# Performance work log

Hardware: AMD Instinct MI355X
Metric: run time of the kernel (lower is better)

Reference implementation:

```python
import jax, jax.numpy as jnp
import numpy as np

B, N, D, H = 32, 2048, 65, 64  # batch, seq_len, in_dim+out_dim, hid
GAMMA = 0.0001


def setup_inputs() -> dict:
    key = jax.random.key(0)
    kx, kq, kk, kv = jax.random.split(key, 4)
    x = jax.random.normal(kx, (B, N, D), dtype=jnp.float32)
    std_qk = (GAMMA / D) ** 0.5
    Wq = jax.random.normal(kq, (H, D), dtype=jnp.float32) * std_qk
    Wk = jax.random.normal(kk, (H, D), dtype=jnp.float32) * std_qk
    Wv = jax.random.normal(kv, (D, D), dtype=jnp.float32) * GAMMA
    return {"x": x, "Wq": Wq, "Wk": Wk, "Wv": Wv}


def reference(x, Wq, Wk, Wv):
    # Linear projections (torch nn.Linear: x @ W^T)
    Q = jnp.einsum('bnd,hd->bnh', x, Wq)  # [B, N, H]
    K = jnp.einsum('bnd,hd->bnh', x, Wk)  # [B, N, H]
    V = jnp.einsum('bnd,ed->bne', x, Wv)  # [B, N, D]
    # Non-softmax linear attention: (Q K^T) V, as written in the module
    scores = jnp.einsum('bnh,bmh->bnm', Q, K)  # [B, N, N]
    out = jnp.einsum('bnm,bmd->bnd', scores, V)  # [B, N, D]
    return out
```

## Files before the change

kernel.cpp:

```cpp
#include <hip/hip_runtime.h>

#define BB 32
#define NN 2048
#define DD 65
#define HH 64
#define ST 68
#define TILE (DD * ST)
#define CC 32

__device__ __forceinline__ float4 f4add(float4 a, float4 b) {
  return make_float4(a.x + b.x, a.y + b.y, a.z + b.z, a.w + b.w);
}

#define GL2LDS(g, l)                                             \
  __builtin_amdgcn_global_load_lds(                              \
      (const __attribute__((address_space(1))) void*)(g),        \
      (__attribute__((address_space(3))) void*)(l), 16, 0, 0)

__global__ __launch_bounds__(256, 4) void k1_gram(const float* __restrict__ x,
                                                  float* __restrict__ P) {
  __shared__ __align__(16) float Xl[64 * ST];
  const int t = (int)threadIdx.x;
  const int tx = t & 15, ty = t >> 4;
  const int blk = (int)blockIdx.x;
  const int b = blk >> 5, c = blk & 31;
  const float4* src4 =
      (const float4*)(x + ((size_t)b * NN + (size_t)c * 64) * DD);

  {
    float4 tmp[5];
#pragma unroll
    for (int q = 0; q < 5; q++) {
      const int i4 = t + 256 * q;
      if (i4 < 1040) tmp[q] = src4[i4];
    }
#pragma unroll
    for (int q = 0; q < 5; q++) {
      const int i4 = t + 256 * q;
      if (i4 < 1040) {
        const int f = 4 * i4;
        const float vv[4] = {tmp[q].x, tmp[q].y, tmp[q].z, tmp[q].w};
#pragma unroll
        for (int j = 0; j < 4; j++) {
          const int r = (f + j) / DD, cc = (f + j) - r * DD;
          Xl[r * ST + cc] = vv[j];
        }
      }
    }
  }
  __syncthreads();

  float g[4][4] = {};
  float g64[4] = {};
  float gcc = 0.f;
  for (int n = 0; n < 64; n++) {
    float rowf[4], colf[4];
    *(float4*)rowf = *(const float4*)&Xl[n * ST + 4 * ty];
    *(float4*)colf = *(const float4*)&Xl[n * ST + 4 * tx];
    const float x64 = Xl[n * ST + 64];
#pragma unroll
    for (int r = 0; r < 4; r++)
#pragma unroll
      for (int cc = 0; cc < 4; cc++)
        g[r][cc] = fmaf(rowf[r], colf[cc], g[r][cc]);
#pragma unroll
    for (int cc = 0; cc < 4; cc++) g64[cc] = fmaf(x64, colf[cc], g64[cc]);
    gcc = fmaf(x64, x64, gcc);
  }
  float* Pp = P + (size_t)blk * TILE;
#pragma unroll
  for (int r = 0; r < 4; r++)
    *(float4*)&Pp[(4 * ty + r) * ST + 4 * tx] = *(float4*)g[r];
  if (ty == 0) {
    *(float4*)&Pp[64 * ST + 4 * tx] = *(float4*)g64;
#pragma unroll
    for (int cc = 0; cc < 4; cc++)
      Pp[(4 * tx + cc) * ST + 64] = g64[cc];
    if (tx == 0) Pp[64 * ST + 64] = gcc;
  }
}

__global__ __launch_bounds__(256) void kred(const float* __restrict__ P,
                                            float* __restrict__ G) {
  const int t = (int)threadIdx.x;
  const int blk = (int)blockIdx.x;
  const int b = blk / 5, s = blk - b * 5;
  const int Q = TILE / 4;
  const int i4 = s * 256 + t;
  if (i4 < Q) {
    const float4* Pb = (const float4*)(P + (size_t)b * CC * TILE);
    float4 acc = make_float4(0.f, 0.f, 0.f, 0.f);
#pragma unroll
    for (int grp = 0; grp < 4; grp++) {
      float4 v[8];
#pragma unroll
      for (int cc = 0; cc < 8; cc++)
        v[cc] = Pb[(size_t)(8 * grp + cc) * Q + i4];
#pragma unroll
      for (int stp = 4; stp >= 1; stp >>= 1)
#pragma unroll
        for (int cc = 0; cc < stp; cc++) v[cc] = f4add(v[cc], v[cc + stp]);
      acc = f4add(acc, v[0]);
    }
    ((float4*)(G + (size_t)b * TILE))[i4] = acc;
  }
}

__global__ __launch_bounds__(256) void k2_chain(
    const float* __restrict__ Wq, const float* __restrict__ Wk,
    const float* __restrict__ Wv, const float* __restrict__ G,
    float* __restrict__ Tm) {
  __shared__ __align__(16) float WqL[HH * ST];
  __shared__ __align__(16) float WkL[HH * ST];
  __shared__ __align__(16) float GL[TILE];
  __shared__ __align__(16) float WvT[TILE];
  __shared__ __align__(16) float Mr[8 * ST];
  __shared__ __align__(16) float Rr[8 * ST];

  const int t = (int)threadIdx.x;
  const int tx = t & 31, ty = t >> 5;
  const int blk = (int)blockIdx.x;
  const int b = blk / 9, rg = blk - b * 9;
  const int i = 8 * rg + ty;
  const bool alive = (i < DD);
  const int ic = alive ? i : 0;

  {
    float tq[17], tk[17];
#pragma unroll
    for (int q = 0; q < 17; q++) {
      const int idx = t + 256 * q;
      if (idx < HH * DD) { tq[q] = Wq[idx]; tk[q] = Wk[idx]; }
    }
#pragma unroll
    for (int q = 0; q < 17; q++) {
      const int idx = t + 256 * q;
      if (idx < HH * DD) {
        const int r = idx / DD, cc = idx - r * DD;
        WqL[r * ST + cc] = tq[q];
        WkL[r * ST + cc] = tk[q];
      }
    }
  }
  {
    const float4* Gb4 = (const float4*)(G + (size_t)b * TILE);
    float4 tG[5];
#pragma unroll
    for (int q = 0; q < 5; q++) {
      const int i4 = t + 256 * q;
      if (i4 < TILE / 4) tG[q] = Gb4[i4];
    }
#pragma unroll
    for (int q = 0; q < 5; q++) {
      const int i4 = t + 256 * q;
      if (i4 < TILE / 4) *((float4*)GL + i4) = tG[q];
    }
  }
  {
    float tv[17];
#pragma unroll
    for (int q = 0; q < 17; q++) {
      const int idx = t + 256 * q;
      if (idx < DD * DD) tv[q] = Wv[idx];
    }
#pragma unroll
    for (int q = 0; q < 17; q++) {
      const int idx = t + 256 * q;
      if (idx < DD * DD) {
        const int j = idx / DD, k = idx - j * DD;
        WvT[k * ST + j] = tv[q];
      }
    }
  }
  __syncthreads();

  {
    float m0 = 0.f, m1 = 0.f, m2 = 0.f;
    for (int h = 0; h < HH; h++) {
      const float wq = WqL[h * ST + ic];
      m0 = fmaf(wq, WkL[h * ST + tx], m0);
      m1 = fmaf(wq, WkL[h * ST + tx + 32], m1);
      m2 = fmaf(wq, WkL[h * ST + 64], m2);
    }
    if (alive) {
      Mr[ty * ST + tx] = m0;
      Mr[ty * ST + tx + 32] = m1;
      if (tx == 0) Mr[ty * ST + 64] = m2;
    }
  }
  __syncthreads();

  {
    float r0 = 0.f, r1 = 0.f, r2 = 0.f;
    for (int k = 0; k < DD; k++) {
      const float mm = Mr[ty * ST + k];
      r0 = fmaf(mm, GL[k * ST + tx], r0);
      r1 = fmaf(mm, GL[k * ST + tx + 32], r1);
      r2 = fmaf(mm, GL[k * ST + 64], r2);
    }
    if (alive) {
      Rr[ty * ST + tx] = r0;
      Rr[ty * ST + tx + 32] = r1;
      if (tx == 0) Rr[ty * ST + 64] = r2;
    }
  }
  __syncthreads();

  {
    float t0 = 0.f, t1 = 0.f, t2 = 0.f;
    for (int k = 0; k < DD; k++) {
      const float rv = Rr[ty * ST + k];
      t0 = fmaf(rv, WvT[k * ST + tx], t0);
      t1 = fmaf(rv, WvT[k * ST + tx + 32], t1);
      t2 = fmaf(rv, WvT[k * ST + 64], t2);
    }
    if (alive) {
      float* Tb = Tm + (size_t)b * TILE + (size_t)i * ST;
      Tb[tx] = t0;
      Tb[tx + 32] = t1;
      if (tx == 0) Tb[64] = t2;
    }
  }
}

__global__ __launch_bounds__(256, 4) void k3_out(const float* __restrict__ x,
                                                 const float* __restrict__ Tt,
                                                 float* __restrict__ out) {
  __shared__ __align__(16) float Tl[TILE];
  __shared__ __align__(16) float Xl[64 * ST];
  const int t = (int)threadIdx.x;
  const int tx = t & 15, ty = t >> 4;
  const int wid = t >> 6, lane = t & 63;
  const int blk = (int)blockIdx.x;
  const int b = blk >> 5;
  const int rb = (blk & 31) * 64;
  const float4* Tg4 = (const float4*)(Tt + (size_t)b * TILE);
  const float4* src4 = (const float4*)(x + ((size_t)b * NN + rb) * DD);

#pragma unroll
  for (int q = 0; q < 4; q++) {
    const int s = q * 256 + wid * 64 + lane;
    GL2LDS(Tg4 + s, Tl + (size_t)(q * 256 + wid * 64) * 4);
  }
  {
    const int s = 1024 + wid * 64 + lane;
    if (s < TILE / 4) GL2LDS(Tg4 + s, Tl + (size_t)(1024 + wid * 64) * 4);
  }

  {
    float4 tmp[5];
#pragma unroll
    for (int q = 0; q < 5; q++) {
      const int i4 = t + 256 * q;
      if (i4 < 1040) tmp[q] = src4[i4];
    }
#pragma unroll
    for (int q = 0; q < 5; q++) {
      const int i4 = t + 256 * q;
      if (i4 < 1040) {
        const int f = 4 * i4;
        const float vv[4] = {tmp[q].x, tmp[q].y, tmp[q].z, tmp[q].w};
#pragma unroll
        for (int j = 0; j < 4; j++) {
          const int r = (f + j) / DD, cc = (f + j) - r * DD;
          Xl[r * ST + cc] = vv[j];
        }
      }
    }
  }
  __syncthreads();

  float o[4][4] = {}, o64[4] = {};
  for (int kk = 0; kk < 64; kk += 4) {
    float xa4[4][4];
    float tb4[4][4];
    float t64e[4];
#pragma unroll
    for (int r = 0; r < 4; r++)
      *(float4*)xa4[r] = *(const float4*)&Xl[(4 * ty + r) * ST + kk];
#pragma unroll
    for (int e = 0; e < 4; e++)
      *(float4*)tb4[e] = *(const float4*)&Tl[(kk + e) * ST + 4 * tx];
#pragma unroll
    for (int e = 0; e < 4; e++) t64e[e] = Tl[(kk + e) * ST + 64];
#pragma unroll
    for (int e = 0; e < 4; e++) {
#pragma unroll
      for (int r = 0; r < 4; r++)
#pragma unroll
        for (int cc = 0; cc < 4; cc++)
          o[r][cc] = fmaf(xa4[r][e], tb4[e][cc], o[r][cc]);
#pragma unroll
      for (int r = 0; r < 4; r++)
        o64[r] = fmaf(xa4[r][e], t64e[e], o64[r]);
    }
  }
  {
    float xs[4];
#pragma unroll
    for (int r = 0; r < 4; r++) xs[r] = Xl[(4 * ty + r) * ST + 64];
    float tb[4];
    *(float4*)tb = *(const float4*)&Tl[64 * ST + 4 * tx];
    const float t64 = Tl[64 * ST + 64];
#pragma unroll
    for (int r = 0; r < 4; r++) {
#pragma unroll
      for (int cc = 0; cc < 4; cc++)
        o[r][cc] = fmaf(xs[r], tb[cc], o[r][cc]);
      o64[r] = fmaf(xs[r], t64, o64[r]);
    }
  }

  __syncthreads();
  float* Ol = Xl;
#pragma unroll
  for (int r = 0; r < 4; r++) {
#pragma unroll
    for (int cc = 0; cc < 4; cc++)
      Ol[(4 * ty + r) * DD + 4 * tx + cc] = o[r][cc];
  }
  if (tx == 0) {
#pragma unroll
    for (int r = 0; r < 4; r++) Ol[(4 * ty + r) * DD + 64] = o64[r];
  }
  __syncthreads();
  {
    float4* ob4 = (float4*)(out + ((size_t)b * NN + rb) * DD);
    const float4* Ol4 = (const float4*)Ol;
#pragma unroll
    for (int q = 0; q < 5; q++) {
      const int i4 = t + 256 * q;
      if (i4 < (64 * DD) / 4) ob4[i4] = Ol4[i4];
    }
  }
}

extern "C" void kernel_launch(void* const* d_in, const int* in_sizes, int n_in,
                              void* d_out, int out_size, void* d_ws,
                              size_t ws_size, hipStream_t stream) {
  const float* x = (const float*)d_in[0];
  const float* Wq = (const float*)d_in[1];
  const float* Wk = (const float*)d_in[2];
  const float* Wv = (const float*)d_in[3];
  float* out = (float*)d_out;

  float* P = (float*)d_ws;
  float* G = P + (size_t)BB * CC * TILE;
  float* Tm = G + (size_t)BB * TILE;

  k1_gram<<<BB * CC, 256, 0, stream>>>(x, P);
  kred<<<BB * 5, 256, 0, stream>>>(P, G);
  k2_chain<<<BB * 9, 256, 0, stream>>>(Wq, Wk, Wv, G, Tm);
  k3_out<<<BB * CC, 256, 0, stream>>>(x, Tm, out);
  (void)in_sizes; (void)n_in; (void)out_size; (void)ws_size;
}
```

Before: 117.2 us.

## Fuse four kernels into one cooperative kernel with grid-wide syncs

Replaces the four separate launches (gram partials, reduction, weight chain, output) with one cooperative kernel of 1024 blocks that uses grid.sync between phases and reuses one shared-memory buffer across phases. The chain phase now reads Wq directly from global and stores Wk/Wv in a narrower-stride LDS buffer to fit the smaller footprint. The aim is to remove launch gaps and tail effects between the dependent kernels. The cost is three grid-wide barriers, the requirement that all 1024 blocks be co-resident, and idle blocks during the small reduction and chain phases. If the cooperative launch fails it falls back to the original four launches.

```diff
diff --git a/kernel.cpp b/kernel.cpp
--- a/kernel.cpp
+++ b/kernel.cpp
@@ -1,4 +1,7 @@
 #include <hip/hip_runtime.h>
+#include <hip/hip_cooperative_groups.h>
+
+namespace cg = cooperative_groups;
 
 #define BB 32
 #define NN 2048
@@ -7,6 +10,12 @@
 #define ST 68
 #define TILE (DD * ST)
 #define CC 32
+#define WST 66
+
+#define OFF1 17680
+#define OFFM 35088
+#define OFFR 37264
+#define SMEM_BYTES 39440
 
 __device__ __forceinline__ float4 f4add(float4 a, float4 b) {
   return make_float4(a.x + b.x, a.y + b.y, a.z + b.z, a.w + b.w);
@@ -16,6 +25,325 @@
   __builtin_amdgcn_global_load_lds(                              \
       (const __attribute__((address_space(1))) void*)(g),        \
       (__attribute__((address_space(3))) void*)(l), 16, 0, 0)
+
+__global__ __launch_bounds__(256, 4) void fused(
+    const float* __restrict__ x, const float* __restrict__ Wq,
+    const float* __restrict__ Wk, const float* __restrict__ Wv,
+    float* __restrict__ P, float* __restrict__ G, float* __restrict__ Tm,
+    float* __restrict__ out) {
+  __shared__ __align__(16) char smem[SMEM_BYTES];
+  const int t = (int)threadIdx.x;
+  const int bid = (int)blockIdx.x;
+
+  {
+    float* Xl = (float*)smem;
+    const int tx = t & 15, ty = t >> 4;
+    const int b = bid >> 5, c = bid & 31;
+    const float4* src4 =
+        (const float4*)(x + ((size_t)b * NN + (size_t)c * 64) * DD);
+
+    {
+      float4 tmp[5];
+#pragma unroll
+      for (int q = 0; q < 5; q++) {
+        const int i4 = t + 256 * q;
+        if (i4 < 1040) tmp[q] = src4[i4];
+      }
+#pragma unroll
+      for (int q = 0; q < 5; q++) {
+        const int i4 = t + 256 * q;
+        if (i4 < 1040) {
+          const int f = 4 * i4;
+          const float vv[4] = {tmp[q].x, tmp[q].y, tmp[q].z, tmp[q].w};
+#pragma unroll
+          for (int j = 0; j < 4; j++) {
+            const int r = (f + j) / DD, cc = (f + j) - r * DD;
+            Xl[r * ST + cc] = vv[j];
+          }
+        }
+      }
+    }
+    __syncthreads();
+
+    float g[4][4] = {};
+    float g64[4] = {};
+    float gcc = 0.f;
+    for (int n = 0; n < 64; n++) {
+      float rowf[4], colf[4];
+      *(float4*)rowf = *(const float4*)&Xl[n * ST + 4 * ty];
+      *(float4*)colf = *(const float4*)&Xl[n * ST + 4 * tx];
+      const float x64 = Xl[n * ST + 64];
+#pragma unroll
+      for (int r = 0; r < 4; r++)
+#pragma unroll
+        for (int cc = 0; cc < 4; cc++)
+          g[r][cc] = fmaf(rowf[r], colf[cc], g[r][cc]);
+#pragma unroll
+      for (int cc = 0; cc < 4; cc++) g64[cc] = fmaf(x64, colf[cc], g64[cc]);
+      gcc = fmaf(x64, x64, gcc);
+    }
+    float* Pp = P + (size_t)bid * TILE;
+#pragma unroll
+    for (int r = 0; r < 4; r++)
+      *(float4*)&Pp[(4 * ty + r) * ST + 4 * tx] = *(float4*)g[r];
+    if (ty == 0) {
+      *(float4*)&Pp[64 * ST + 4 * tx] = *(float4*)g64;
+#pragma unroll
+      for (int cc = 0; cc < 4; cc++)
+        Pp[(4 * tx + cc) * ST + 64] = g64[cc];
+      if (tx == 0) Pp[64 * ST + 64] = gcc;
+    }
+  }
+  cg::this_grid().sync();
+
+  if (bid < BB * 5) {
+    const int b = bid / 5, s = bid - b * 5;
+    const int Q = TILE / 4;
+    const int i4 = s * 256 + t;
+    if (i4 < Q) {
+      const float4* Pb = (const float4*)(P + (size_t)b * CC * TILE);
+      float4 acc = make_float4(0.f, 0.f, 0.f, 0.f);
+#pragma unroll
+      for (int grp = 0; grp < 4; grp++) {
+        float4 v[8];
+#pragma unroll
+        for (int cc = 0; cc < 8; cc++)
+          v[cc] = Pb[(size_t)(8 * grp + cc) * Q + i4];
+#pragma unroll
+        for (int stp = 4; stp >= 1; stp >>= 1)
+#pragma unroll
+          for (int cc = 0; cc < stp; cc++) v[cc] = f4add(v[cc], v[cc + stp]);
+        acc = f4add(acc, v[0]);
+      }
+      ((float4*)(G + (size_t)b * TILE))[i4] = acc;
+    }
+  }
+  cg::this_grid().sync();
+
+  if (bid < BB * 9) {
+    float* GL = (float*)smem;
+    float* WkL = (float*)(smem + OFF1);
+    float* Mr = (float*)(smem + OFFM);
+    float* Rr = (float*)(smem + OFFR);
+    const int tx = t & 31, ty = t >> 5;
+    const int b = bid / 9, rg = bid - b * 9;
+    const int i = 8 * rg + ty;
+    const bool alive = (i < DD);
+    const int ic = alive ? i : 0;
+
+    {
+      const float4* Wk4 = (const float4*)Wk;
+      const float4* Gb4 = (const float4*)(G + (size_t)b * TILE);
+      float4 tk[5], tG[5];
+#pragma unroll
+      for (int q = 0; q < 5; q++) {
+        const int i4 = t + 256 * q;
+        if (i4 < 1040) tk[q] = Wk4[i4];
+      }
+#pragma unroll
+      for (int q = 0; q < 5; q++) {
+        const int i4 = t + 256 * q;
+        if (i4 < TILE / 4) tG[q] = Gb4[i4];
+      }
+#pragma unroll
+      for (int q = 0; q < 5; q++) {
+        const int i4 = t + 256 * q;
+        if (i4 < 1040) {
+          const int f = 4 * i4;
+          const float vv[4] = {tk[q].x, tk[q].y, tk[q].z, tk[q].w};
+#pragma unroll
+          for (int j = 0; j < 4; j++) {
+            const int r = (f + j) / DD, cc = (f + j) - r * DD;
+            WkL[r * WST + cc] = vv[j];
+          }
+        }
+      }
+#pragma unroll
+      for (int q = 0; q < 5; q++) {
+        const int i4 = t + 256 * q;
+        if (i4 < TILE / 4) ((float4*)GL)[i4] = tG[q];
+      }
+    }
+    __syncthreads();
+
+    {
+      float m0 = 0.f, m1 = 0.f, m2 = 0.f;
+#pragma unroll 4
+      for (int h = 0; h < HH; h++) {
+        const float wq = Wq[h * DD + ic];
+        m0 = fmaf(wq, WkL[h * WST + tx], m0);
+        m1 = fmaf(wq, WkL[h * WST + tx + 32], m1);
+        m2 = fmaf(wq, WkL[h * WST + 64], m2);
+      }
+      if (alive) {
+        Mr[ty * ST + tx] = m0;
+        Mr[ty * ST + tx + 32] = m1;
+        if (tx == 0) Mr[ty * ST + 64] = m2;
+      }
+    }
+    __syncthreads();
+
+    {
+      float r0 = 0.f, r1 = 0.f, r2 = 0.f;
+      for (int k = 0; k < DD; k++) {
+        const float mm = Mr[ty * ST + k];
+        r0 = fmaf(mm, GL[k * ST + tx], r0);
+        r1 = fmaf(mm, GL[k * ST + tx + 32], r1);
+        r2 = fmaf(mm, GL[k * ST + 64], r2);
+      }
+      if (alive) {
+        Rr[ty * ST + tx] = r0;
+        Rr[ty * ST + tx + 32] = r1;
+        if (tx == 0) Rr[ty * ST + 64] = r2;
+      }
+    }
+    __syncthreads();
+
+    {
+      float tv[17];
+#pragma unroll
+      for (int q = 0; q < 17; q++) {
+        const int idx = t + 256 * q;
+        if (idx < DD * DD) tv[q] = Wv[idx];
+      }
+#pragma unroll
+      for (int q = 0; q < 17; q++) {
+        const int idx = t + 256 * q;
+        if (idx < DD * DD) {
+          const int j = idx / DD, k = idx - j * DD;
+          WkL[k * WST + j] = tv[q];
+        }
+      }
+    }
+    __syncthreads();
+
+    {
+      const float* WvT = WkL;
+      float t0 = 0.f, t1 = 0.f, t2 = 0.f;
+      for (int k = 0; k < DD; k++) {
+        const float rv = Rr[ty * ST + k];
+        t0 = fmaf(rv, WvT[k * WST + tx], t0);
+        t1 = fmaf(rv, WvT[k * WST + tx + 32], t1);
+        t2 = fmaf(rv, WvT[k * WST + 64], t2);
+      }
+      if (alive) {
+        float* Tb = Tm + (size_t)b * TILE + (size_t)i * ST;
+        Tb[tx] = t0;
+        Tb[tx + 32] = t1;
+        if (tx == 0) Tb[64] = t2;
+      }
+    }
+  }
+  cg::this_grid().sync();
+
+  {
+    float* Tl = (float*)smem;
+    float* Xl = (float*)(smem + OFF1);
+    const int tx = t & 15, ty = t >> 4;
+    const int wid = t >> 6, lane = t & 63;
+    const int b = bid >> 5;
+    const int rb = (bid & 31) * 64;
+    const float4* Tg4 = (const float4*)(Tm + (size_t)b * TILE);
+    const float4* src4 = (const float4*)(x + ((size_t)b * NN + rb) * DD);
+
+#pragma unroll
+    for (int q = 0; q < 4; q++) {
+      const int s = q * 256 + wid * 64 + lane;
+      GL2LDS(Tg4 + s, Tl + (size_t)(q * 256 + wid * 64) * 4);
+    }
+    {
+      const int s = 1024 + wid * 64 + lane;
+      if (s < TILE / 4) GL2LDS(Tg4 + s, Tl + (size_t)(1024 + wid * 64) * 4);
+    }
+
+    {
+      float4 tmp[5];
+#pragma unroll
+      for (int q = 0; q < 5; q++) {
+        const int i4 = t + 256 * q;
+        if (i4 < 1040) tmp[q] = src4[i4];
+      }
+#pragma unroll
+      for (int q = 0; q < 5; q++) {
+        const int i4 = t + 256 * q;
+        if (i4 < 1040) {
+          const int f = 4 * i4;
+          const float vv[4] = {tmp[q].x, tmp[q].y, tmp[q].z, tmp[q].w};
+#pragma unroll
+          for (int j = 0; j < 4; j++) {
+            const int r = (f + j) / DD, cc = (f + j) - r * DD;
+            Xl[r * ST + cc] = vv[j];
+          }
+        }
+      }
+    }
+    __syncthreads();
+
+    float o[4][4] = {}, o64[4] = {};
+    for (int kk = 0; kk < 64; kk += 4) {
+      float xa4[4][4];
+      float tb4[4][4];
+      float t64e[4];
+#pragma unroll
+      for (int r = 0; r < 4; r++)
+        *(float4*)xa4[r] = *(const float4*)&Xl[(4 * ty + r) * ST + kk];
+#pragma unroll
+      for (int e = 0; e < 4; e++)
+        *(float4*)tb4[e] = *(const float4*)&Tl[(kk + e) * ST + 4 * tx];
+#pragma unroll
+      for (int e = 0; e < 4; e++) t64e[e] = Tl[(kk + e) * ST + 64];
+#pragma unroll
+      for (int e = 0; e < 4; e++) {
+#pragma unroll
+        for (int r = 0; r < 4; r++)
+#pragma unroll
+          for (int cc = 0; cc < 4; cc++)
+            o[r][cc] = fmaf(xa4[r][e], tb4[e][cc], o[r][cc]);
+#pragma unroll
+        for (int r = 0; r < 4; r++)
+          o64[r] = fmaf(xa4[r][e], t64e[e], o64[r]);
+      }
+    }
+    {
+      float xs[4];
+#pragma unroll
+      for (int r = 0; r < 4; r++) xs[r] = Xl[(4 * ty + r) * ST + 64];
+      float tb[4];
+      *(float4*)tb = *(const float4*)&Tl[64 * ST + 4 * tx];
+      const float t64 = Tl[64 * ST + 64];
+#pragma unroll
+      for (int r = 0; r < 4; r++) {
+#pragma unroll
+        for (int cc = 0; cc < 4; cc++)
+          o[r][cc] = fmaf(xs[r], tb[cc], o[r][cc]);
+        o64[r] = fmaf(xs[r], t64, o64[r]);
+      }
+    }
+
+    __syncthreads();
+    float* Ol = Xl;
+#pragma unroll
+    for (int r = 0; r < 4; r++) {
+#pragma unroll
+      for (int cc = 0; cc < 4; cc++)
+        Ol[(4 * ty + r) * DD + 4 * tx + cc] = o[r][cc];
+    }
+    if (tx == 0) {
+#pragma unroll
+      for (int r = 0; r < 4; r++) Ol[(4 * ty + r) * DD + 64] = o64[r];
+    }
+    __syncthreads();
+    {
+      float4* ob4 = (float4*)(out + ((size_t)b * NN + rb) * DD);
+      const float4* Ol4 = (const float4*)Ol;
+#pragma unroll
+      for (int q = 0; q < 5; q++) {
+        const int i4 = t + 256 * q;
+        if (i4 < (64 * DD) / 4) ob4[i4] = Ol4[i4];
+      }
+    }
+  }
+}
 
 __global__ __launch_bounds__(256, 4) void k1_gram(const float* __restrict__ x,
                                                   float* __restrict__ P) {
@@ -26,7 +354,6 @@
   const int b = blk >> 5, c = blk & 31;
   const float4* src4 =
       (const float4*)(x + ((size_t)b * NN + (size_t)c * 64) * DD);
-
   {
     float4 tmp[5];
 #pragma unroll
@@ -49,9 +376,7 @@
     }
   }
   __syncthreads();
-
-  float g[4][4] = {};
-  float g64[4] = {};
+  float g[4][4] = {}, g64[4] = {};
   float gcc = 0.f;
   for (int n = 0; n < 64; n++) {
     float rowf[4], colf[4];
@@ -74,8 +399,7 @@
   if (ty == 0) {
     *(float4*)&Pp[64 * ST + 4 * tx] = *(float4*)g64;
 #pragma unroll
-    for (int cc = 0; cc < 4; cc++)
-      Pp[(4 * tx + cc) * ST + 64] = g64[cc];
+    for (int cc = 0; cc < 4; cc++) Pp[(4 * tx + cc) * ST + 64] = g64[cc];
     if (tx == 0) Pp[64 * ST + 64] = gcc;
   }
 }
@@ -116,7 +440,6 @@
   __shared__ __align__(16) float WvT[TILE];
   __shared__ __align__(16) float Mr[8 * ST];
   __shared__ __align__(16) float Rr[8 * ST];
-
   const int t = (int)threadIdx.x;
   const int tx = t & 31, ty = t >> 5;
   const int blk = (int)blockIdx.x;
@@ -124,7 +447,6 @@
   const int i = 8 * rg + ty;
   const bool alive = (i < DD);
   const int ic = alive ? i : 0;
-
   {
     float tq[17], tk[17];
 #pragma unroll
@@ -173,7 +495,6 @@
     }
   }
   __syncthreads();
-
   {
     float m0 = 0.f, m1 = 0.f, m2 = 0.f;
     for (int h = 0; h < HH; h++) {
@@ -189,7 +510,6 @@
     }
   }
   __syncthreads();
-
   {
     float r0 = 0.f, r1 = 0.f, r2 = 0.f;
     for (int k = 0; k < DD; k++) {
@@ -205,7 +525,6 @@
     }
   }
   __syncthreads();
-
   {
     float t0 = 0.f, t1 = 0.f, t2 = 0.f;
     for (int k = 0; k < DD; k++) {
@@ -236,7 +555,6 @@
   const int rb = (blk & 31) * 64;
   const float4* Tg4 = (const float4*)(Tt + (size_t)b * TILE);
   const float4* src4 = (const float4*)(x + ((size_t)b * NN + rb) * DD);
-
 #pragma unroll
   for (int q = 0; q < 4; q++) {
     const int s = q * 256 + wid * 64 + lane;
@@ -246,7 +564,6 @@
     const int s = 1024 + wid * 64 + lane;
     if (s < TILE / 4) GL2LDS(Tg4 + s, Tl + (size_t)(1024 + wid * 64) * 4);
   }
-
   {
     float4 tmp[5];
 #pragma unroll
@@ -269,12 +586,9 @@
     }
   }
   __syncthreads();
-
   float o[4][4] = {}, o64[4] = {};
   for (int kk = 0; kk < 64; kk += 4) {
-    float xa4[4][4];
-    float tb4[4][4];
-    float t64e[4];
+    float xa4[4][4], tb4[4][4], t64e[4];
 #pragma unroll
     for (int r = 0; r < 4; r++)
       *(float4*)xa4[r] = *(const float4*)&Xl[(4 * ty + r) * ST + kk];
@@ -310,7 +624,6 @@
       o64[r] = fmaf(xs[r], t64, o64[r]);
     }
   }
-
   __syncthreads();
   float* Ol = Xl;
 #pragma unroll
@@ -348,9 +661,15 @@
   float* G = P + (size_t)BB * CC * TILE;
   float* Tm = G + (size_t)BB * TILE;
 
-  k1_gram<<<BB * CC, 256, 0, stream>>>(x, P);
-  kred<<<BB * 5, 256, 0, stream>>>(P, G);
-  k2_chain<<<BB * 9, 256, 0, stream>>>(Wq, Wk, Wv, G, Tm);
-  k3_out<<<BB * CC, 256, 0, stream>>>(x, Tm, out);
+  void* kargs[] = {(void*)&x, (void*)&Wq, (void*)&Wk, (void*)&Wv,
+                   (void*)&P, (void*)&G, (void*)&Tm, (void*)&out};
+  hipError_t err = hipLaunchCooperativeKernel(
+      (void*)fused, dim3(BB * CC), dim3(256), kargs, 0, stream);
+  if (err != hipSuccess) {
+    k1_gram<<<BB * CC, 256, 0, stream>>>(x, P);
+    kred<<<BB * 5, 256, 0, stream>>>(P, G);
+    k2_chain<<<BB * 9, 256, 0, stream>>>(Wq, Wk, Wv, G, Tm);
+    k3_out<<<BB * CC, 256, 0, stream>>>(x, Tm, out);
+  }
   (void)in_sizes; (void)n_in; (void)out_size; (void)ws_size;
 }
```

Result: slower. 419.8 us (+258.3%).

## Fuse gram reduction and weight chain into gram kernel via last-block atomic counter

Applied to the files above, without the earlier changes.

Merges the partial-gram, reduction and Wq/Wk/Wv chain kernels into one kernel. The last block per batch, detected with a threadfence plus an atomic counter, sums the 32 partial grams and computes the 65x65 chain product with a 4x4 register tile per thread. This removes two kernel launches and the G round trip through global memory. In exchange, the serial tail of each batch now runs on a single block, and an extra memset launch is added to reset the counters.

```diff
diff --git a/kernel.cpp b/kernel.cpp
--- a/kernel.cpp
+++ b/kernel.cpp
@@ -17,215 +17,247 @@
       (const __attribute__((address_space(1))) void*)(g),        \
       (__attribute__((address_space(3))) void*)(l), 16, 0, 0)
 
-__global__ __launch_bounds__(256, 4) void k1_gram(const float* __restrict__ x,
-                                                  float* __restrict__ P) {
-  __shared__ __align__(16) float Xl[64 * ST];
+__global__ __launch_bounds__(256, 4) void kA(
+    const float* __restrict__ x, const float* __restrict__ Wq,
+    const float* __restrict__ Wk, const float* __restrict__ Wv,
+    float* __restrict__ P, float* __restrict__ Tm, int* __restrict__ cnt) {
+  __shared__ __align__(16) float smem[2 * TILE];
+  __shared__ int s_last;
+  float* R0f = smem;
+  float* R1f = smem + TILE;
   const int t = (int)threadIdx.x;
   const int tx = t & 15, ty = t >> 4;
   const int blk = (int)blockIdx.x;
   const int b = blk >> 5, c = blk & 31;
-  const float4* src4 =
-      (const float4*)(x + ((size_t)b * NN + (size_t)c * 64) * DD);
-
-  {
-    float4 tmp[5];
-#pragma unroll
-    for (int q = 0; q < 5; q++) {
-      const int i4 = t + 256 * q;
-      if (i4 < 1040) tmp[q] = src4[i4];
+
+  {
+    float* Xl = R0f;
+    const float4* src4 =
+        (const float4*)(x + ((size_t)b * NN + (size_t)c * 64) * DD);
+    {
+      float4 tmp[5];
+#pragma unroll
+      for (int q = 0; q < 5; q++) {
+        const int i4 = t + 256 * q;
+        if (i4 < 1040) tmp[q] = src4[i4];
+      }
+#pragma unroll
+      for (int q = 0; q < 5; q++) {
+        const int i4 = t + 256 * q;
+        if (i4 < 1040) {
+          const int f = 4 * i4;
+          const float vv[4] = {tmp[q].x, tmp[q].y, tmp[q].z, tmp[q].w};
+#pragma unroll
+          for (int j = 0; j < 4; j++) {
+            const int r = (f + j) / DD, cc = (f + j) - r * DD;
+            Xl[r * ST + cc] = vv[j];
+          }
+        }
+      }
+    }
+    __syncthreads();
+
+    float g[4][4] = {};
+    float g64[4] = {};
+    float gcc = 0.f;
+    for (int n = 0; n < 64; n++) {
+      float rowf[4], colf[4];
+      *(float4*)rowf = *(const float4*)&Xl[n * ST + 4 * ty];
+      *(float4*)colf = *(const float4*)&Xl[n * ST + 4 * tx];
+      const float x64 = Xl[n * ST + 64];
+#pragma unroll
+      for (int r = 0; r < 4; r++)
+#pragma unroll
+        for (int cc = 0; cc < 4; cc++)
+          g[r][cc] = fmaf(rowf[r], colf[cc], g[r][cc]);
+#pragma unroll
+      for (int cc = 0; cc < 4; cc++) g64[cc] = fmaf(x64, colf[cc], g64[cc]);
+      gcc = fmaf(x64, x64, gcc);
+    }
+    float* Pp = P + (size_t)blk * TILE;
+#pragma unroll
+    for (int r = 0; r < 4; r++)
+      *(float4*)&Pp[(4 * ty + r) * ST + 4 * tx] = *(float4*)g[r];
+    if (ty == 0) {
+      *(float4*)&Pp[64 * ST + 4 * tx] = *(float4*)g64;
+#pragma unroll
+      for (int cc = 0; cc < 4; cc++)
+        Pp[(4 * tx + cc) * ST + 64] = g64[cc];
+      if (tx == 0) Pp[64 * ST + 64] = gcc;
+    }
+  }
+
+  __threadfence();
+  __syncthreads();
+  if (t == 0) s_last = atomicAdd(&cnt[b], 1);
+  __syncthreads();
+  if (s_last != CC - 1) return;
+  __threadfence();
+
+  {
+    const float4* Pb = (const float4*)(P + (size_t)b * CC * TILE);
+    const int Q = TILE / 4;
+#pragma unroll
+    for (int q = 0; q < 5; q++) {
+      const int i4 = t + 256 * q;
+      if (i4 < Q) {
+        float4 acc = make_float4(0.f, 0.f, 0.f, 0.f);
+#pragma unroll
+        for (int grp = 0; grp < 4; grp++) {
+          float4 v[8];
+#pragma unroll
+          for (int cc = 0; cc < 8; cc++)
+            v[cc] = Pb[(size_t)(8 * grp + cc) * Q + i4];
+#pragma unroll
+          for (int stp = 4; stp >= 1; stp >>= 1)
+#pragma unroll
+            for (int cc = 0; cc < stp; cc++)
+              v[cc] = f4add(v[cc], v[cc + stp]);
+          acc = f4add(acc, v[0]);
+        }
+        ((float4*)R0f)[i4] = acc;
+      }
+    }
+  }
+  {
+    const float4* Wk4 = (const float4*)Wk;
+    float4 tk[5];
+#pragma unroll
+    for (int q = 0; q < 5; q++) {
+      const int i4 = t + 256 * q;
+      if (i4 < 1040) tk[q] = Wk4[i4];
     }
 #pragma unroll
     for (int q = 0; q < 5; q++) {
       const int i4 = t + 256 * q;
       if (i4 < 1040) {
         const int f = 4 * i4;
-        const float vv[4] = {tmp[q].x, tmp[q].y, tmp[q].z, tmp[q].w};
+        const float vv[4] = {tk[q].x, tk[q].y, tk[q].z, tk[q].w};
 #pragma unroll
         for (int j = 0; j < 4; j++) {
           const int r = (f + j) / DD, cc = (f + j) - r * DD;
-          Xl[r * ST + cc] = vv[j];
+          R1f[r * ST + cc] = vv[j];
         }
       }
     }
   }
   __syncthreads();
 
-  float g[4][4] = {};
-  float g64[4] = {};
-  float gcc = 0.f;
-  for (int n = 0; n < 64; n++) {
-    float rowf[4], colf[4];
-    *(float4*)rowf = *(const float4*)&Xl[n * ST + 4 * ty];
-    *(float4*)colf = *(const float4*)&Xl[n * ST + 4 * tx];
-    const float x64 = Xl[n * ST + 64];
+  float m[4][4] = {}, mrow[4] = {}, mcol[4] = {};
+  float mcc = 0.f;
+  for (int h = 0; h < HH; h++) {
+    float kb[4];
+    *(float4*)kb = *(const float4*)&R1f[h * ST + 4 * tx];
+    const float k64 = R1f[h * ST + 64];
+    float qa[4];
+#pragma unroll
+    for (int r = 0; r < 4; r++) qa[r] = Wq[h * DD + 4 * ty + r];
+    const float q64 = Wq[h * DD + 64];
+#pragma unroll
+    for (int r = 0; r < 4; r++)
+#pragma unroll
+      for (int cc = 0; cc < 4; cc++) m[r][cc] = fmaf(qa[r], kb[cc], m[r][cc]);
+#pragma unroll
+    for (int cc = 0; cc < 4; cc++) mrow[cc] = fmaf(q64, kb[cc], mrow[cc]);
+#pragma unroll
+    for (int r = 0; r < 4; r++) mcol[r] = fmaf(qa[r], k64, mcol[r]);
+    mcc = fmaf(q64, k64, mcc);
+  }
+  __syncthreads();
+#pragma unroll
+  for (int r = 0; r < 4; r++)
+    *(float4*)&R1f[(4 * ty + r) * ST + 4 * tx] = *(float4*)m[r];
+  if (ty == 0) *(float4*)&R1f[64 * ST + 4 * tx] = *(float4*)mrow;
+  if (tx == 0) {
+#pragma unroll
+    for (int r = 0; r < 4; r++) R1f[(4 * ty + r) * ST + 64] = mcol[r];
+    if (ty == 0) R1f[64 * ST + 64] = mcc;
+  }
+  __syncthreads();
+
+  float rr[4][4] = {}, r64j[4] = {}, ri64[4] = {};
+  float rcc = 0.f;
+  for (int k = 0; k < DD; k++) {
+    float gb[4];
+    *(float4*)gb = *(const float4*)&R0f[k * ST + 4 * tx];
+    const float g64 = R0f[k * ST + 64];
+    float ma[4];
+#pragma unroll
+    for (int r = 0; r < 4; r++) ma[r] = R1f[(4 * ty + r) * ST + k];
+    const float m64 = R1f[64 * ST + k];
 #pragma unroll
     for (int r = 0; r < 4; r++)
 #pragma unroll
       for (int cc = 0; cc < 4; cc++)
-        g[r][cc] = fmaf(rowf[r], colf[cc], g[r][cc]);
-#pragma unroll
-    for (int cc = 0; cc < 4; cc++) g64[cc] = fmaf(x64, colf[cc], g64[cc]);
-    gcc = fmaf(x64, x64, gcc);
-  }
-  float* Pp = P + (size_t)blk * TILE;
+        rr[r][cc] = fmaf(ma[r], gb[cc], rr[r][cc]);
+#pragma unroll
+    for (int cc = 0; cc < 4; cc++) r64j[cc] = fmaf(m64, gb[cc], r64j[cc]);
+#pragma unroll
+    for (int r = 0; r < 4; r++) ri64[r] = fmaf(ma[r], g64, ri64[r]);
+    rcc = fmaf(m64, g64, rcc);
+  }
+  float tv[17];
+#pragma unroll
+  for (int q = 0; q < 17; q++) {
+    const int idx = t + 256 * q;
+    if (idx < DD * DD) tv[q] = Wv[idx];
+  }
+  __syncthreads();
 #pragma unroll
   for (int r = 0; r < 4; r++)
-    *(float4*)&Pp[(4 * ty + r) * ST + 4 * tx] = *(float4*)g[r];
-  if (ty == 0) {
-    *(float4*)&Pp[64 * ST + 4 * tx] = *(float4*)g64;
-#pragma unroll
-    for (int cc = 0; cc < 4; cc++)
-      Pp[(4 * tx + cc) * ST + 64] = g64[cc];
-    if (tx == 0) Pp[64 * ST + 64] = gcc;
+    *(float4*)&R1f[(4 * ty + r) * ST + 4 * tx] = *(float4*)rr[r];
+  if (ty == 0) *(float4*)&R1f[64 * ST + 4 * tx] = *(float4*)r64j;
+  if (tx == 0) {
+#pragma unroll
+    for (int r = 0; r < 4; r++) R1f[(4 * ty + r) * ST + 64] = ri64[r];
+    if (ty == 0) R1f[64 * ST + 64] = rcc;
+  }
+#pragma unroll
+  for (int q = 0; q < 17; q++) {
+    const int idx = t + 256 * q;
+    if (idx < DD * DD) {
+      const int j = idx / DD, k = idx - j * DD;
+      R0f[k * ST + j] = tv[q];
+    }
+  }
+  __syncthreads();
+
+  float tt[4][4] = {}, row64[4] = {}, col64[4] = {};
+  float tcc = 0.f;
+  for (int k = 0; k < DD; k++) {
+    float wv[4];
+    *(float4*)wv = *(const float4*)&R0f[k * ST + 4 * tx];
+    const float w64 = R0f[k * ST + 64];
+    float ra[4];
+#pragma unroll
+    for (int r = 0; r < 4; r++) ra[r] = R1f[(4 * ty + r) * ST + k];
+    const float r64 = R1f[64 * ST + k];
+#pragma unroll
+    for (int r = 0; r < 4; r++)
+#pragma unroll
+      for (int cc = 0; cc < 4; cc++)
+        tt[r][cc] = fmaf(ra[r], wv[cc], tt[r][cc]);
+#pragma unroll
+    for (int cc = 0; cc < 4; cc++) row64[cc] = fmaf(r64, wv[cc], row64[cc]);
+#pragma unroll
+    for (int r = 0; r < 4; r++) col64[r] = fmaf(ra[r], w64, col64[r]);
+    tcc = fmaf(r64, w64, tcc);
+  }
+  float* Tb = Tm + (size_t)b * TILE;
+#pragma unroll
+  for (int r = 0; r < 4; r++)
+    *(float4*)&Tb[(4 * ty + r) * ST + 4 * tx] = *(float4*)tt[r];
+  if (ty == 0) *(float4*)&Tb[64 * ST + 4 * tx] = *(float4*)row64;
+  if (tx == 0) {
+#pragma unroll
+    for (int r = 0; r < 4; r++) Tb[(4 * ty + r) * ST + 64] = col64[r];
+    if (ty == 0) Tb[64 * ST + 64] = tcc;
   }
 }
 
-__global__ __launch_bounds__(256) void kred(const float* __restrict__ P,
-                                            float* __restrict__ G) {
-  const int t = (int)threadIdx.x;
-  const int blk = (int)blockIdx.x;
-  const int b = blk / 5, s = blk - b * 5;
-  const int Q = TILE / 4;
-  const int i4 = s * 256 + t;
-  if (i4 < Q) {
-    const float4* Pb = (const float4*)(P + (size_t)b * CC * TILE);
-    float4 acc = make_float4(0.f, 0.f, 0.f, 0.f);
-#pragma unroll
-    for (int grp = 0; grp < 4; grp++) {
-      float4 v[8];
-#pragma unroll
-      for (int cc = 0; cc < 8; cc++)
-        v[cc] = Pb[(size_t)(8 * grp + cc) * Q + i4];
-#pragma unroll
-      for (int stp = 4; stp >= 1; stp >>= 1)
-#pragma unroll
-        for (int cc = 0; cc < stp; cc++) v[cc] = f4add(v[cc], v[cc + stp]);
-      acc = f4add(acc, v[0]);
-    }
-    ((float4*)(G + (size_t)b * TILE))[i4] = acc;
-  }
-}
-
-__global__ __launch_bounds__(256) void k2_chain(
-    const float* __restrict__ Wq, const float* __restrict__ Wk,
-    const float* __restrict__ Wv, const float* __restrict__ G,
-    float* __restrict__ Tm) {
-  __shared__ __align__(16) float WqL[HH * ST];
-  __shared__ __align__(16) float WkL[HH * ST];
-  __shared__ __align__(16) float GL[TILE];
-  __shared__ __align__(16) float WvT[TILE];
-  __shared__ __align__(16) float Mr[8 * ST];
-  __shared__ __align__(16) float Rr[8 * ST];
-
-  const int t = (int)threadIdx.x;
-  const int tx = t & 31, ty = t >> 5;
-  const int blk = (int)blockIdx.x;
-  const int b = blk / 9, rg = blk - b * 9;
-  const int i = 8 * rg + ty;
-  const bool alive = (i < DD);
-  const int ic = alive ? i : 0;
-
-  {
-    float tq[17], tk[17];
-#pragma unroll
-    for (int q = 0; q < 17; q++) {
-      const int idx = t + 256 * q;
-      if (idx < HH * DD) { tq[q] = Wq[idx]; tk[q] = Wk[idx]; }
-    }
-#pragma unroll
-    for (int q = 0; q < 17; q++) {
-      const int idx = t + 256 * q;
-      if (idx < HH * DD) {
-        const int r = idx / DD, cc = idx - r * DD;
-        WqL[r * ST + cc] = tq[q];
-        WkL[r * ST + cc] = tk[q];
-      }
-    }
-  }
-  {
-    const float4* Gb4 = (const float4*)(G + (size_t)b * TILE);
-    float4 tG[5];
-#pragma unroll
-    for (int q = 0; q < 5; q++) {
-      const int i4 = t + 256 * q;
-      if (i4 < TILE / 4) tG[q] = Gb4[i4];
-    }
-#pragma unroll
-    for (int q = 0; q < 5; q++) {
-      const int i4 = t + 256 * q;
-      if (i4 < TILE / 4) *((float4*)GL + i4) = tG[q];
-    }
-  }
-  {
-    float tv[17];
-#pragma unroll
-    for (int q = 0; q < 17; q++) {
-      const int idx = t + 256 * q;
-      if (idx < DD * DD) tv[q] = Wv[idx];
-    }
-#pragma unroll
-    for (int q = 0; q < 17; q++) {
-      const int idx = t + 256 * q;
-      if (idx < DD * DD) {
-        const int j = idx / DD, k = idx - j * DD;
-        WvT[k * ST + j] = tv[q];
-      }
-    }
-  }
-  __syncthreads();
-
-  {
-    float m0 = 0.f, m1 = 0.f, m2 = 0.f;
-    for (int h = 0; h < HH; h++) {
-      const float wq = WqL[h * ST + ic];
-      m0 = fmaf(wq, WkL[h * ST + tx], m0);
-      m1 = fmaf(wq, WkL[h * ST + tx + 32], m1);
-      m2 = fmaf(wq, WkL[h * ST + 64], m2);
-    }
-    if (alive) {
-      Mr[ty * ST + tx] = m0;
-      Mr[ty * ST + tx + 32] = m1;
-      if (tx == 0) Mr[ty * ST + 64] = m2;
-    }
-  }
-  __syncthreads();
-
-  {
-    float r0 = 0.f, r1 = 0.f, r2 = 0.f;
-    for (int k = 0; k < DD; k++) {
-      const float mm = Mr[ty * ST + k];
-      r0 = fmaf(mm, GL[k * ST + tx], r0);
-      r1 = fmaf(mm, GL[k * ST + tx + 32], r1);
-      r2 = fmaf(mm, GL[k * ST + 64], r2);
-    }
-    if (alive) {
-      Rr[ty * ST + tx] = r0;
-      Rr[ty * ST + tx + 32] = r1;
-      if (tx == 0) Rr[ty * ST + 64] = r2;
-    }
-  }
-  __syncthreads();
-
-  {
-    float t0 = 0.f, t1 = 0.f, t2 = 0.f;
-    for (int k = 0; k < DD; k++) {
-      const float rv = Rr[ty * ST + k];
-      t0 = fmaf(rv, WvT[k * ST + tx], t0);
-      t1 = fmaf(rv, WvT[k * ST + tx + 32], t1);
-      t2 = fmaf(rv, WvT[k * ST + 64], t2);
-    }
-    if (alive) {
-      float* Tb = Tm + (size_t)b * TILE + (size_t)i * ST;
-      Tb[tx] = t0;
-      Tb[tx + 32] = t1;
-      if (tx == 0) Tb[64] = t2;
-    }
-  }
-}
-
-__global__ __launch_bounds__(256, 4) void k3_out(const float* __restrict__ x,
-                                                 const float* __restrict__ Tt,
-                                                 float* __restrict__ out) {
+__global__ __launch_bounds__(256, 4) void kB(const float* __restrict__ x,
+                                             const float* __restrict__ Tt,
+                                             float* __restrict__ out) {
   __shared__ __align__(16) float Tl[TILE];
   __shared__ __align__(16) float Xl[64 * ST];
   const int t = (int)threadIdx.x;
@@ -246,7 +278,6 @@
     const int s = 1024 + wid * 64 + lane;
     if (s < TILE / 4) GL2LDS(Tg4 + s, Tl + (size_t)(1024 + wid * 64) * 4);
   }
-
   {
     float4 tmp[5];
 #pragma unroll
@@ -272,9 +303,7 @@
 
   float o[4][4] = {}, o64[4] = {};
   for (int kk = 0; kk < 64; kk += 4) {
-    float xa4[4][4];
-    float tb4[4][4];
-    float t64e[4];
+    float xa4[4][4], tb4[4][4], t64e[4];
 #pragma unroll
     for (int r = 0; r < 4; r++)
       *(float4*)xa4[r] = *(const float4*)&Xl[(4 * ty + r) * ST + kk];
@@ -345,12 +374,11 @@
   float* out = (float*)d_out;
 
   float* P = (float*)d_ws;
-  float* G = P + (size_t)BB * CC * TILE;
-  float* Tm = G + (size_t)BB * TILE;
-
-  k1_gram<<<BB * CC, 256, 0, stream>>>(x, P);
-  kred<<<BB * 5, 256, 0, stream>>>(P, G);
-  k2_chain<<<BB * 9, 256, 0, stream>>>(Wq, Wk, Wv, G, Tm);
-  k3_out<<<BB * CC, 256, 0, stream>>>(x, Tm, out);
+  float* Tm = P + (size_t)BB * CC * TILE;
+  int* cnt = (int*)(Tm + (size_t)BB * TILE);
+
+  hipMemsetAsync(cnt, 0, BB * sizeof(int), stream);
+  kA<<<BB * CC, 256, 0, stream>>>(x, Wq, Wk, Wv, P, Tm, cnt);
+  kB<<<BB * CC, 256, 0, stream>>>(x, Tm, out);
   (void)in_sizes; (void)n_in; (void)out_size; (void)ws_size;
 }
```

Result: slower. 282.1 us (+140.7%).

## Split reduction dimension across warps with 8x8 register tiles and LDS reduction

Applied to the files above, without the earlier changes.

In both the Gram kernel and the output kernel, each 64-lane wavefront now takes a quarter of the reduction dimension and computes a full 64x64 tile with 8x8 register blocks. Partial sums from wavefronts 1-3 are then reduced into wavefront 0 through LDS. The aim is more FMAs per LDS load, since each thread loads 8+8 values for 64 FMAs instead of 4+4 for 16. The cost is a serialized three-step LDS reduction with extra barriers, an extra LDS buffer in k1, and higher register pressure under launch_bounds(256,4).

```diff
diff --git a/kernel.cpp b/kernel.cpp
--- a/kernel.cpp
+++ b/kernel.cpp
@@ -20,8 +20,10 @@
 __global__ __launch_bounds__(256, 4) void k1_gram(const float* __restrict__ x,
                                                   float* __restrict__ P) {
   __shared__ __align__(16) float Xl[64 * ST];
+  __shared__ __align__(16) float Buf[TILE];
   const int t = (int)threadIdx.x;
-  const int tx = t & 15, ty = t >> 4;
+  const int w = t >> 6, lane = t & 63;
+  const int tx8 = lane & 7, ty8 = lane >> 3;
   const int blk = (int)blockIdx.x;
   const int b = blk >> 5, c = blk & 31;
   const float4* src4 =
@@ -50,33 +52,74 @@
   }
   __syncthreads();
 
-  float g[4][4] = {};
-  float g64[4] = {};
+  float g[8][8] = {};
+  float f64[8] = {};
   float gcc = 0.f;
-  for (int n = 0; n < 64; n++) {
-    float rowf[4], colf[4];
-    *(float4*)rowf = *(const float4*)&Xl[n * ST + 4 * ty];
-    *(float4*)colf = *(const float4*)&Xl[n * ST + 4 * tx];
+  for (int n = 16 * w; n < 16 * w + 16; n++) {
+    float rowf[8], colf[8];
+    *(float4*)&rowf[0] = *(const float4*)&Xl[n * ST + 8 * ty8];
+    *(float4*)&rowf[4] = *(const float4*)&Xl[n * ST + 8 * ty8 + 4];
+    *(float4*)&colf[0] = *(const float4*)&Xl[n * ST + 8 * tx8];
+    *(float4*)&colf[4] = *(const float4*)&Xl[n * ST + 8 * tx8 + 4];
     const float x64 = Xl[n * ST + 64];
 #pragma unroll
-    for (int r = 0; r < 4; r++)
-#pragma unroll
-      for (int cc = 0; cc < 4; cc++)
+    for (int r = 0; r < 8; r++)
+#pragma unroll
+      for (int cc = 0; cc < 8; cc++)
         g[r][cc] = fmaf(rowf[r], colf[cc], g[r][cc]);
 #pragma unroll
-    for (int cc = 0; cc < 4; cc++) g64[cc] = fmaf(x64, colf[cc], g64[cc]);
+    for (int cc = 0; cc < 8; cc++) f64[cc] = fmaf(x64, colf[cc], f64[cc]);
     gcc = fmaf(x64, x64, gcc);
   }
-  float* Pp = P + (size_t)blk * TILE;
-#pragma unroll
-  for (int r = 0; r < 4; r++)
-    *(float4*)&Pp[(4 * ty + r) * ST + 4 * tx] = *(float4*)g[r];
-  if (ty == 0) {
-    *(float4*)&Pp[64 * ST + 4 * tx] = *(float4*)g64;
-#pragma unroll
-    for (int cc = 0; cc < 4; cc++)
-      Pp[(4 * tx + cc) * ST + 64] = g64[cc];
-    if (tx == 0) Pp[64 * ST + 64] = gcc;
+  __syncthreads();
+
+#pragma unroll 1
+  for (int srcw = 1; srcw < 4; srcw++) {
+    if (w == srcw) {
+#pragma unroll
+      for (int r = 0; r < 8; r++) {
+        *(float4*)&Buf[(8 * ty8 + r) * ST + 8 * tx8] = *(float4*)&g[r][0];
+        *(float4*)&Buf[(8 * ty8 + r) * ST + 8 * tx8 + 4] = *(float4*)&g[r][4];
+      }
+      if (ty8 == 0) {
+#pragma unroll
+        for (int cc = 0; cc < 8; cc++) Buf[64 * ST + 8 * tx8 + cc] = f64[cc];
+        if (tx8 == 0) Buf[64 * ST + 64] = gcc;
+      }
+    }
+    __syncthreads();
+    if (w == 0) {
+#pragma unroll
+      for (int r = 0; r < 8; r++) {
+        float pa[8];
+        *(float4*)&pa[0] = *(const float4*)&Buf[(8 * ty8 + r) * ST + 8 * tx8];
+        *(float4*)&pa[4] =
+            *(const float4*)&Buf[(8 * ty8 + r) * ST + 8 * tx8 + 4];
+#pragma unroll
+        for (int cc = 0; cc < 8; cc++) g[r][cc] += pa[cc];
+      }
+#pragma unroll
+      for (int cc = 0; cc < 8; cc++) f64[cc] += Buf[64 * ST + 8 * tx8 + cc];
+      gcc += Buf[64 * ST + 64];
+    }
+    __syncthreads();
+  }
+
+  if (w == 0) {
+    float* Pp = P + (size_t)blk * TILE;
+#pragma unroll
+    for (int r = 0; r < 8; r++) {
+      *(float4*)&Pp[(8 * ty8 + r) * ST + 8 * tx8] = *(float4*)&g[r][0];
+      *(float4*)&Pp[(8 * ty8 + r) * ST + 8 * tx8 + 4] = *(float4*)&g[r][4];
+    }
+    if (ty8 == 0) {
+#pragma unroll
+      for (int cc = 0; cc < 8; cc++) {
+        Pp[64 * ST + 8 * tx8 + cc] = f64[cc];
+        Pp[(8 * tx8 + cc) * ST + 64] = f64[cc];
+      }
+      if (tx8 == 0) Pp[64 * ST + 64] = gcc;
+    }
   }
 }
 
@@ -229,8 +272,8 @@
   __shared__ __align__(16) float Tl[TILE];
   __shared__ __align__(16) float Xl[64 * ST];
   const int t = (int)threadIdx.x;
-  const int tx = t & 15, ty = t >> 4;
-  const int wid = t >> 6, lane = t & 63;
+  const int w = t >> 6, lane = t & 63;
+  const int tx8 = lane & 7, ty8 = lane >> 3;
   const int blk = (int)blockIdx.x;
   const int b = blk >> 5;
   const int rb = (blk & 31) * 64;
@@ -239,14 +282,13 @@
 
 #pragma unroll
   for (int q = 0; q < 4; q++) {
-    const int s = q * 256 + wid * 64 + lane;
-    GL2LDS(Tg4 + s, Tl + (size_t)(q * 256 + wid * 64) * 4);
-  }
-  {
-    const int s = 1024 + wid * 64 + lane;
-    if (s < TILE / 4) GL2LDS(Tg4 + s, Tl + (size_t)(1024 + wid * 64) * 4);
-  }
-
+    const int s = q * 256 + w * 64 + lane;
+    GL2LDS(Tg4 + s, Tl + (size_t)(q * 256 + w * 64) * 4);
+  }
+  {
+    const int s = 1024 + w * 64 + lane;
+    if (s < TILE / 4) GL2LDS(Tg4 + s, Tl + (size_t)(1024 + w * 64) * 4);
+  }
   {
     float4 tmp[5];
 #pragma unroll
@@ -270,58 +312,90 @@
   }
   __syncthreads();
 
-  float o[4][4] = {}, o64[4] = {};
-  for (int kk = 0; kk < 64; kk += 4) {
-    float xa4[4][4];
-    float tb4[4][4];
-    float t64e[4];
-#pragma unroll
-    for (int r = 0; r < 4; r++)
-      *(float4*)xa4[r] = *(const float4*)&Xl[(4 * ty + r) * ST + kk];
-#pragma unroll
-    for (int e = 0; e < 4; e++)
-      *(float4*)tb4[e] = *(const float4*)&Tl[(kk + e) * ST + 4 * tx];
-#pragma unroll
-    for (int e = 0; e < 4; e++) t64e[e] = Tl[(kk + e) * ST + 64];
+  float o[8][8] = {}, o64[8] = {};
+  const int kbase = 16 * w;
+  for (int kk = kbase; kk < kbase + 16; kk += 4) {
+    float4 xr[8];
+#pragma unroll
+    for (int r = 0; r < 8; r++)
+      xr[r] = *(const float4*)&Xl[(8 * ty8 + r) * ST + kk];
+    const float* xe[4] = {&xr[0].x, 0, 0, 0};
+    (void)xe;
 #pragma unroll
     for (int e = 0; e < 4; e++) {
-#pragma unroll
-      for (int r = 0; r < 4; r++)
-#pragma unroll
-        for (int cc = 0; cc < 4; cc++)
-          o[r][cc] = fmaf(xa4[r][e], tb4[e][cc], o[r][cc]);
-#pragma unroll
-      for (int r = 0; r < 4; r++)
-        o64[r] = fmaf(xa4[r][e], t64e[e], o64[r]);
-    }
-  }
-  {
-    float xs[4];
-#pragma unroll
-    for (int r = 0; r < 4; r++) xs[r] = Xl[(4 * ty + r) * ST + 64];
-    float tb[4];
-    *(float4*)tb = *(const float4*)&Tl[64 * ST + 4 * tx];
+      const int k = kk + e;
+      float tb[8];
+      *(float4*)&tb[0] = *(const float4*)&Tl[k * ST + 8 * tx8];
+      *(float4*)&tb[4] = *(const float4*)&Tl[k * ST + 8 * tx8 + 4];
+      const float t64 = Tl[k * ST + 64];
+#pragma unroll
+      for (int r = 0; r < 8; r++) {
+        const float xv = (e == 0) ? xr[r].x
+                       : (e == 1) ? xr[r].y
+                       : (e == 2) ? xr[r].z : xr[r].w;
+#pragma unroll
+        for (int cc = 0; cc < 8; cc++)
+          o[r][cc] = fmaf(xv, tb[cc], o[r][cc]);
+        o64[r] = fmaf(xv, t64, o64[r]);
+      }
+    }
+  }
+  if (w == 3) {
+    float tb[8];
+    *(float4*)&tb[0] = *(const float4*)&Tl[64 * ST + 8 * tx8];
+    *(float4*)&tb[4] = *(const float4*)&Tl[64 * ST + 8 * tx8 + 4];
     const float t64 = Tl[64 * ST + 64];
 #pragma unroll
-    for (int r = 0; r < 4; r++) {
-#pragma unroll
-      for (int cc = 0; cc < 4; cc++)
-        o[r][cc] = fmaf(xs[r], tb[cc], o[r][cc]);
-      o64[r] = fmaf(xs[r], t64, o64[r]);
-    }
-  }
-
-  __syncthreads();
+    for (int r = 0; r < 8; r++) {
+      const float xv = Xl[(8 * ty8 + r) * ST + 64];
+#pragma unroll
+      for (int cc = 0; cc < 8; cc++)
+        o[r][cc] = fmaf(xv, tb[cc], o[r][cc]);
+      o64[r] = fmaf(xv, t64, o64[r]);
+    }
+  }
+  __syncthreads();
+
+  float* Buf = Xl;
+#pragma unroll 1
+  for (int srcw = 1; srcw < 4; srcw++) {
+    if (w == srcw) {
+#pragma unroll
+      for (int r = 0; r < 8; r++) {
+        *(float4*)&Buf[(8 * ty8 + r) * ST + 8 * tx8] = *(float4*)&o[r][0];
+        *(float4*)&Buf[(8 * ty8 + r) * ST + 8 * tx8 + 4] = *(float4*)&o[r][4];
+      }
+      if (tx8 == 0) {
+#pragma unroll
+        for (int r = 0; r < 8; r++) Buf[(8 * ty8 + r) * ST + 64] = o64[r];
+      }
+    }
+    __syncthreads();
+    if (w == 0) {
+#pragma unroll
+      for (int r = 0; r < 8; r++) {
+        float pa[8];
+        *(float4*)&pa[0] = *(const float4*)&Buf[(8 * ty8 + r) * ST + 8 * tx8];
+        *(float4*)&pa[4] =
+            *(const float4*)&Buf[(8 * ty8 + r) * ST + 8 * tx8 + 4];
+#pragma unroll
+        for (int cc = 0; cc < 8; cc++) o[r][cc] += pa[cc];
+        o64[r] += Buf[(8 * ty8 + r) * ST + 64];
+      }
+    }
+    __syncthreads();
+  }
+
   float* Ol = Xl;
-#pragma unroll
-  for (int r = 0; r < 4; r++) {
-#pragma unroll
-    for (int cc = 0; cc < 4; cc++)
-      Ol[(4 * ty + r) * DD + 4 * tx + cc] = o[r][cc];
-  }
-  if (tx == 0) {
-#pragma unroll
-    for (int r = 0; r < 4; r++) Ol[(4 * ty + r) * DD + 64] = o64[r];
+  if (w == 0) {
+#pragma unroll
+    for (int r = 0; r < 8; r++) {
+      const int row = 8 * ty8 + r;
+#pragma unroll
+      for (int cc = 0; cc < 8; cc++)
+        Ol[row * DD + 8 * tx8 + cc] = o[r][cc];
+      if (tx8 == 0) Ol[row * DD + 64] = o64[r];
+    }
   }
   __syncthreads();
   {
```

After: 123.8 us. 5.7% more time.
